# Kernel optimization log

Measured on AMD Instinct MI355X. Metric: run time of the kernel, lower is better.

Reference implementation:

```python
import jax, jax.numpy as jnp
import numpy as np

B, C, D_EMB = 512, 100000, 128
SCALE = 3.0
EPS = 1e-5


def _l2norm(x, eps=1e-12):
    # matches torch F.normalize(p=2, dim=-1)
    n = jnp.sqrt(jnp.sum(x * x, axis=-1, keepdims=True))
    return x / jnp.maximum(n, eps)


def setup_inputs() -> dict:
    key = jax.random.key(0)
    k1, k2, k3 = jax.random.split(key, 3)
    X = jax.random.normal(k1, (B, D_EMB), dtype=jnp.float32)
    indices = jnp.arange(B, dtype=jnp.int64)
    T = jax.random.randint(k2, (B,), 0, C).astype(jnp.int64)
    proxies = jax.random.normal(k3, (C, D_EMB), dtype=jnp.float32) / 8.0
    return {"X": X, "indices": indices, "T": T, "proxies": proxies}


def reference(X, indices, T, proxies):
    P = _l2norm(proxies)            # (C, D)
    Xn = _l2norm(X)                 # (B, D)

    # cross_attention -----------------------------------------------------
    Pb = P[T]                       # (B, D) gather of class proxies
    # affinity2boundary[b,k] = relu(<(Pb[b]+Pb[k])/2, Xn[k]>)
    #   = relu(0.5 * ((Pb @ Xn.T)[b,k] + diag[k]))  -- avoids (B,B,D) intermediate
    diag = jnp.sum(Pb * Xn, axis=-1)                       # (B,)
    aff2b = jax.nn.relu(0.5 * (Pb @ Xn.T + diag[None, :]))  # (B, B)
    aff2x = jax.nn.relu(Xn @ Xn.T)                          # (B, B)
    attention = aff2b + aff2x

    # NOTE: faithful to torch broadcasting: (B,B) / (B,) divides by COLUMN sums
    attention = attention / (attention.sum(-1) + EPS)       # (B, B)
    attention_weights = attention @ Xn                      # (B, D)
    X2 = Xn + attention_weights

    Ps = SCALE * _l2norm(P)         # (C, D), rows have norm SCALE
    Xs = SCALE * _l2norm(X2)        # (B, D)

    # squared pairwise distance block between X rows and proxy rows
    sx = jnp.sum(Xs * Xs, axis=-1)  # (B,)
    sp = jnp.sum(Ps * Ps, axis=-1)  # (C,)
    Dm = jnp.maximum(sx[:, None] + sp[None, :] - 2.0 * (Xs @ Ps.T), 0.0)  # (B, C)

    # one-hot targets (smoothing_const = 0) with masked log-softmax
    lsm = jax.nn.log_softmax(-Dm, axis=-1)                  # (B, C)
    loss = -lsm[jnp.arange(B), T]                           # (B,)
    return loss.mean()
```

## Files before the change

### kernel.cpp

```cpp
#include <hip/hip_runtime.h>
#include <hip/hip_bf16.h>
#include <math.h>

#define B_N 512
#define C_N 100000
#define CPAD 100032
#define D_N 128
#define NCHUNK (CPAD / 64)
#define K5_BLOCKS (CPAD / 4)
#define K6_GX 256
#define K6_GY 4
#define K6_BLOCKS (K6_GX * K6_GY)
#define PAD_CORR (32.0f * 1.522998e-8f)

typedef short short8 __attribute__((ext_vector_type(8)));
typedef float f32x4 __attribute__((ext_vector_type(4)));

__device__ __forceinline__ unsigned short f2bf(float f) {
  unsigned int u = __float_as_uint(f);
  u += 0x7fffu + ((u >> 16) & 1u);
  return (unsigned short)(u >> 16);
}

__device__ __forceinline__ void gl_lds16(const void* g, void* l) {
  __builtin_amdgcn_global_load_lds(
      (const __attribute__((address_space(1))) void*)g,
      (__attribute__((address_space(3))) void*)l, 16, 0, 0);
}

template <int NT>
__device__ __forceinline__ float block_reduce_sum(float v, float* red) {
  int t = threadIdx.x;
  __syncthreads();
  red[t] = v;
  __syncthreads();
#pragma unroll
  for (int s = NT / 2; s > 0; s >>= 1) {
    if (t < s) red[t] += red[t + s];
    __syncthreads();
  }
  return red[0];
}

__global__ __launch_bounds__(256) void kA(const float* __restrict__ X,
                                          const float* __restrict__ proxies,
                                          const int* __restrict__ T,
                                          float* __restrict__ Xn, float* __restrict__ Pb,
                                          float* __restrict__ diagv, float* __restrict__ X2,
                                          unsigned short* __restrict__ Pnb) {
  int bid = blockIdx.x;
  int t = threadIdx.x;
  if (bid < K5_BLOCKS) {
    int lane = t & 63;
    int row = bid * 4 + (t >> 6);
    float2 v = make_float2(0.f, 0.f);
    if (row < C_N) v = *(const float2*)(proxies + (size_t)row * D_N + 2 * lane);
    float ss = v.x * v.x + v.y * v.y;
#pragma unroll
    for (int off = 1; off < 64; off <<= 1) ss += __shfl_xor(ss, off);
    float inv = 1.f / fmaxf(sqrtf(ss), 1e-12f);
    unsigned short a = f2bf(v.x * inv), b = f2bf(v.y * inv);
    unsigned int pk = (unsigned int)a | ((unsigned int)b << 16);
    *(unsigned int*)(Pnb + (size_t)row * D_N + 2 * lane) = pk;
  } else {
    __shared__ float red[256];
    int b = bid - K5_BLOCKS;
    bool act = t < D_N;
    float v = act ? X[b * D_N + t] : 0.f;
    float ss = block_reduce_sum<256>(v * v, red);
    float xn = v / fmaxf(sqrtf(ss), 1e-12f);
    if (act) {
      Xn[b * D_N + t] = xn;
      X2[b * D_N + t] = 0.f;
    }
    int row = T[b];
    float p = act ? proxies[(size_t)row * D_N + t] : 0.f;
    float ss2 = block_reduce_sum<256>(p * p, red);
    float pn = p / fmaxf(sqrtf(ss2), 1e-12f);
    if (act) Pb[b * D_N + t] = pn;
    float d = block_reduce_sum<256>(pn * xn, red);
    if (t == 0) diagv[b] = d;
  }
}

__global__ __launch_bounds__(256) void k3_att(const float* __restrict__ Xn,
                                              const float* __restrict__ Pb,
                                              const float* __restrict__ diagv,
                                              float* __restrict__ A, float* __restrict__ S) {
  __shared__ float xb[128], pbv[128];
  __shared__ float red[256];
  int b = blockIdx.x, t = threadIdx.x;
  if (t < 128) {
    xb[t] = Xn[b * D_N + t];
    pbv[t] = Pb[b * D_N + t];
  }
  __syncthreads();
  float rs = 0.f;
  for (int k = t; k < B_N; k += 256) {
    const float4* xr = (const float4*)(Xn + (size_t)k * D_N);
    float d1 = 0.f, d2 = 0.f;
#pragma unroll
    for (int i = 0; i < 32; i++) {
      float4 v = xr[i];
      d1 += pbv[4 * i] * v.x + pbv[4 * i + 1] * v.y + pbv[4 * i + 2] * v.z + pbv[4 * i + 3] * v.w;
      d2 += xb[4 * i] * v.x + xb[4 * i + 1] * v.y + xb[4 * i + 2] * v.z + xb[4 * i + 3] * v.w;
    }
    float a = fmaxf(0.5f * (d1 + diagv[k]), 0.f) + fmaxf(d2, 0.f);
    A[(size_t)b * B_N + k] = a;
    rs += a;
  }
  rs = block_reduce_sum<256>(rs, red);
  if (t == 0) S[b] = rs;
}

__global__ void k4a_aw(const float* __restrict__ Xn, const float* __restrict__ A,
                       const float* __restrict__ S, float* __restrict__ X2) {
  __shared__ float aw[128];
  int b = blockIdx.x, t = threadIdx.x;
  int k0 = blockIdx.y * 128;
  aw[t] = A[(size_t)b * B_N + k0 + t] / (S[k0 + t] + 1e-5f);
  __syncthreads();
  float acc = 0.f;
#pragma unroll 16
  for (int kk = 0; kk < 128; kk++) acc += aw[kk] * Xn[(size_t)(k0 + kk) * D_N + t];
  atomicAdd(&X2[b * D_N + t], acc);
}

__global__ void k4b_xs(const float* __restrict__ Xn, const float* __restrict__ X2,
                       const float* __restrict__ Pb, unsigned short* __restrict__ Xsb,
                       float* __restrict__ lossT, float* __restrict__ sumexpP,
                       int* __restrict__ ctrs) {
  __shared__ float red[128];
  int b = blockIdx.x, t = threadIdx.x;
  float x2 = Xn[b * D_N + t] + X2[b * D_N + t];
  float ss = block_reduce_sum<128>(x2 * x2, red);
  float xs = 3.f * x2 / fmaxf(sqrtf(ss), 1e-12f);
  Xsb[b * D_N + t] = f2bf(xs);
  float dt = block_reduce_sum<128>(xs * Pb[b * D_N + t], red);
  if (t == 0) {
    lossT[b] = fmaxf(18.f - 6.f * dt, 0.f);
    sumexpP[b * 16] = 0.f;
    if (b == 0) ctrs[32] = 0;
  }
}

__global__ __launch_bounds__(256, 4) void k6_big(const unsigned short* __restrict__ Pnb,
                                                 const unsigned short* __restrict__ Xsb,
                                                 float* __restrict__ sumexpP,
                                                 const float* __restrict__ lossT,
                                                 int* __restrict__ ctrs,
                                                 float* __restrict__ out) {
  __shared__ __align__(16) unsigned short sP[2][64 * 128];
  __shared__ float redf[256];
  const int t = threadIdx.x;
  const int w = t >> 6;
  const int lane = t & 63;
  const int lc = lane & 15;
  const int q = lane >> 4;
  const int b0 = blockIdx.y * 128;

  short8 afr[2][4];
#pragma unroll
  for (int mt = 0; mt < 2; mt++)
#pragma unroll
    for (int ks = 0; ks < 4; ks++)
      afr[mt][ks] = *(const short8*)(Xsb + (size_t)(b0 + 32 * w + 16 * mt + lc) * D_N +
                                     ks * 32 + q * 8);

  float pe[2][4];
#pragma unroll
  for (int mt = 0; mt < 2; mt++)
#pragma unroll
    for (int r = 0; r < 4; r++) pe[mt][r] = 0.f;

  const int rR = 16 * w + (lane >> 4);
  const int gsrc0 = (lane & 15);
#define STAGE(c0_, buf_)                                                              \
  {                                                                                   \
    _Pragma("unroll") for (int j = 0; j < 4; j++) {                                   \
      int R = rR + 4 * j;                                                             \
      int g = gsrc0 ^ ((R)&15);                                                       \
      gl_lds16(Pnb + (((size_t)(c0_) + R) << 7) + (g << 3),                           \
               &sP[buf_][w * 2048 + j * 512]);                                        \
    }                                                                                 \
  }

  int cc = blockIdx.x;
  STAGE(cc * 64, 0);
  int buf = 0;
  while (true) {
    __syncthreads();
    int nc = cc + gridDim.x;
    if (nc < NCHUNK) STAGE(nc * 64, buf ^ 1);

    f32x4 acc[2][4];
#pragma unroll
    for (int mt = 0; mt < 2; mt++)
#pragma unroll
      for (int nt = 0; nt < 4; nt++) acc[mt][nt] = (f32x4){0.f, 0.f, 0.f, 0.f};

#pragma unroll
    for (int ks = 0; ks < 4; ks++) {
      short8 bfr[4];
#pragma unroll
      for (int nt = 0; nt < 4; nt++) {
        int R = 16 * nt + lc;
        int g = (ks * 4 + q) ^ lc;
        bfr[nt] = *(const short8*)(&sP[buf][R * 128 + (g << 3)]);
      }
#pragma unroll
      for (int nt = 0; nt < 4; nt++)
#pragma unroll
        for (int mt = 0; mt < 2; mt++)
          acc[mt][nt] = __builtin_amdgcn_mfma_f32_16x16x32_bf16(afr[mt][ks], bfr[nt],
                                                                acc[mt][nt], 0, 0, 0);
    }

#pragma unroll
    for (int mt = 0; mt < 2; mt++)
#pragma unroll
      for (int nt = 0; nt < 4; nt++) {
        f32x4 a = acc[mt][nt];
#pragma unroll
        for (int r = 0; r < 4; r++)
          pe[mt][r] += __expf(fminf(6.f * a[r] - 18.f, 0.f));
      }
    if (nc >= NCHUNK) break;
    cc = nc;
    buf ^= 1;
  }

#pragma unroll
  for (int mt = 0; mt < 2; mt++) {
#pragma unroll
    for (int r = 0; r < 4; r++) {
      float p = pe[mt][r];
      p += __shfl_xor(p, 1);
      p += __shfl_xor(p, 2);
      p += __shfl_xor(p, 4);
      p += __shfl_xor(p, 8);
      if (lc == 0) {
        int rb = b0 + 32 * w + 16 * mt + 4 * q + r;
        atomicAdd(&sumexpP[rb * 16], p);
      }
    }
  }

  __builtin_amdgcn_s_waitcnt(0);
  __shared__ int sLast;
  if (t == 0) sLast = atomicAdd(&ctrs[32], 1);
  __syncthreads();
  if (sLast == K6_BLOCKS - 1) {
    float v = 0.f;
#pragma unroll
    for (int i = 0; i < 2; i++) {
      int b = t + 256 * i;
      float se = __hip_atomic_load(&sumexpP[b * 16], __ATOMIC_RELAXED,
                                   __HIP_MEMORY_SCOPE_AGENT);
      v += lossT[b] + logf(se - PAD_CORR);
    }
    float s = block_reduce_sum<256>(v, redf);
    if (t == 0) out[0] = s * (1.0f / 512.0f);
  }
}

extern "C" void kernel_launch(void* const* d_in, const int* in_sizes, int n_in,
                              void* d_out, int out_size, void* d_ws, size_t ws_size,
                              hipStream_t stream) {
  const float* X = (const float*)d_in[0];
  const int* T = (const int*)d_in[2];
  const float* proxies = (const float*)d_in[3];
  float* out = (float*)d_out;

  char* ws = (char*)d_ws;
  unsigned short* Pnb = (unsigned short*)ws;
  float* Xn = (float*)(ws + (size_t)CPAD * D_N * 2);
  float* Pb = Xn + B_N * D_N;
  float* X2 = Pb + B_N * D_N;
  float* dg = X2 + B_N * D_N;
  float* S = dg + B_N;
  float* lossT = S + B_N;
  float* sumexpP = lossT + B_N;
  unsigned short* Xsb = (unsigned short*)(sumexpP + B_N * 16);
  float* A = (float*)(Xsb + B_N * D_N);
  int* ctrs = (int*)(A + B_N * B_N);

  kA<<<K5_BLOCKS + B_N, 256, 0, stream>>>(X, proxies, T, Xn, Pb, dg, X2, Pnb);
  k3_att<<<B_N, 256, 0, stream>>>(Xn, Pb, dg, A, S);
  k4a_aw<<<dim3(B_N, 4), 128, 0, stream>>>(Xn, A, S, X2);
  k4b_xs<<<B_N, 128, 0, stream>>>(Xn, X2, Pb, Xsb, lossT, sumexpP, ctrs);
  k6_big<<<dim3(K6_GX, K6_GY), 256, 0, stream>>>(Pnb, Xsb, sumexpP, lossT, ctrs, out);
}
```

Before: 161.3 us.

## Load proxy tiles directly from global into registers instead of LDS staging

Removes the double-buffered global_load_lds staging of proxy chunks and the per-chunk barriers in the big distance/softmax kernel. Each wave now loads its B fragments straight from global memory into registers and issues the MFMAs without synchronisation. The four waves of a block read the same proxy chunk, so the change relies on L1/L2 to serve those repeated loads instead of LDS reuse. Launch bounds occupancy drops from 4 to 3 blocks to allow for the larger register footprint.

```diff
diff --git a/kernel.cpp b/kernel.cpp
--- a/kernel.cpp
+++ b/kernel.cpp
@@ -20,12 +20,6 @@
   unsigned int u = __float_as_uint(f);
   u += 0x7fffu + ((u >> 16) & 1u);
   return (unsigned short)(u >> 16);
-}
-
-__device__ __forceinline__ void gl_lds16(const void* g, void* l) {
-  __builtin_amdgcn_global_load_lds(
-      (const __attribute__((address_space(1))) void*)g,
-      (__attribute__((address_space(3))) void*)l, 16, 0, 0);
 }
 
 template <int NT>
@@ -144,14 +138,14 @@
   }
 }
 
-__global__ __launch_bounds__(256, 4) void k6_big(const unsigned short* __restrict__ Pnb,
+__global__ __launch_bounds__(256, 3) void k6_big(const unsigned short* __restrict__ Pnb,
                                                  const unsigned short* __restrict__ Xsb,
                                                  float* __restrict__ sumexpP,
                                                  const float* __restrict__ lossT,
                                                  int* __restrict__ ctrs,
                                                  float* __restrict__ out) {
-  __shared__ __align__(16) unsigned short sP[2][64 * 128];
   __shared__ float redf[256];
+  __shared__ int sLast;
   const int t = threadIdx.x;
   const int w = t >> 6;
   const int lane = t & 63;
@@ -173,25 +167,17 @@
 #pragma unroll
     for (int r = 0; r < 4; r++) pe[mt][r] = 0.f;
 
-  const int rR = 16 * w + (lane >> 4);
-  const int gsrc0 = (lane & 15);
-#define STAGE(c0_, buf_)                                                              \
-  {                                                                                   \
-    _Pragma("unroll") for (int j = 0; j < 4; j++) {                                   \
-      int R = rR + 4 * j;                                                             \
-      int g = gsrc0 ^ ((R)&15);                                                       \
-      gl_lds16(Pnb + (((size_t)(c0_) + R) << 7) + (g << 3),                           \
-               &sP[buf_][w * 2048 + j * 512]);                                        \
-    }                                                                                 \
-  }
-
-  int cc = blockIdx.x;
-  STAGE(cc * 64, 0);
-  int buf = 0;
-  while (true) {
-    __syncthreads();
-    int nc = cc + gridDim.x;
-    if (nc < NCHUNK) STAGE(nc * 64, buf ^ 1);
+  const int boff = lc * D_N + q * 8;
+
+  for (int cc = blockIdx.x; cc < NCHUNK; cc += K6_GX) {
+    const unsigned short* bp = Pnb + ((size_t)cc << 13);
+
+    short8 bfr[4][4];
+#pragma unroll
+    for (int ks = 0; ks < 4; ks++)
+#pragma unroll
+      for (int nt = 0; nt < 4; nt++)
+        bfr[ks][nt] = *(const short8*)(bp + boff + nt * (16 * D_N) + ks * 32);
 
     f32x4 acc[2][4];
 #pragma unroll
@@ -200,21 +186,14 @@
       for (int nt = 0; nt < 4; nt++) acc[mt][nt] = (f32x4){0.f, 0.f, 0.f, 0.f};
 
 #pragma unroll
-    for (int ks = 0; ks < 4; ks++) {
-      short8 bfr[4];
+    for (int ks = 0; ks < 4; ks++)
 #pragma unroll
       for (int nt = 0; nt < 4; nt++) {
-        int R = 16 * nt + lc;
-        int g = (ks * 4 + q) ^ lc;
-        bfr[nt] = *(const short8*)(&sP[buf][R * 128 + (g << 3)]);
+        acc[0][nt] = __builtin_amdgcn_mfma_f32_16x16x32_bf16(afr[0][ks], bfr[ks][nt],
+                                                             acc[0][nt], 0, 0, 0);
+        acc[1][nt] = __builtin_amdgcn_mfma_f32_16x16x32_bf16(afr[1][ks], bfr[ks][nt],
+                                                             acc[1][nt], 0, 0, 0);
       }
-#pragma unroll
-      for (int nt = 0; nt < 4; nt++)
-#pragma unroll
-        for (int mt = 0; mt < 2; mt++)
-          acc[mt][nt] = __builtin_amdgcn_mfma_f32_16x16x32_bf16(afr[mt][ks], bfr[nt],
-                                                                acc[mt][nt], 0, 0, 0);
-    }
 
 #pragma unroll
     for (int mt = 0; mt < 2; mt++)
@@ -225,9 +204,6 @@
         for (int r = 0; r < 4; r++)
           pe[mt][r] += __expf(fminf(6.f * a[r] - 18.f, 0.f));
       }
-    if (nc >= NCHUNK) break;
-    cc = nc;
-    buf ^= 1;
   }
 
 #pragma unroll
@@ -247,7 +223,6 @@
   }
 
   __builtin_amdgcn_s_waitcnt(0);
-  __shared__ int sLast;
   if (t == 0) sLast = atomicAdd(&ctrs[32], 1);
   __syncthreads();
   if (sLast == K6_BLOCKS - 1) {
```

Result: slower. 191.6 us (+18.8%).
